# Performance work log

Measured on AMD Instinct MI355X. Metric: run time of the kernel, lower is better.

The kernel has to match this reference:

```python
import jax, jax.numpy as jnp
import numpy as np

NUM_HEADS = 32
NUM_KV_HEADS = 8
HEAD_DIM = 64
GQA_GROUPS = NUM_HEADS // NUM_KV_HEADS
HIDDEN = 2048
B, S = 2, 2048


def setup_inputs() -> dict:
    key = jax.random.key(0)
    ks = jax.random.split(key, 7)
    scale = 1.0 / np.sqrt(HIDDEN)
    return {
        "x": jax.random.normal(ks[0], (B, S, HIDDEN), dtype=jnp.float32),
        "rotary_cos": jax.random.uniform(ks[1], (S, HEAD_DIM // 2), dtype=jnp.float32),
        "rotary_sin": jax.random.uniform(ks[2], (S, HEAD_DIM // 2), dtype=jnp.float32),
        "Wq": jax.random.normal(ks[3], (HIDDEN, NUM_HEADS * HEAD_DIM), dtype=jnp.float32) * scale,
        "Wk": jax.random.normal(ks[4], (HIDDEN, NUM_KV_HEADS * HEAD_DIM), dtype=jnp.float32) * scale,
        "Wv": jax.random.normal(ks[5], (HIDDEN, NUM_KV_HEADS * HEAD_DIM), dtype=jnp.float32) * scale,
        "Wo": jax.random.normal(ks[6], (NUM_HEADS * HEAD_DIM, HIDDEN), dtype=jnp.float32) * scale,
    }


def _apply_rope(x, cos, sin):
    # x: (B, H, S, hd); cos/sin: (S, hd/2)
    d = x.shape[-1] // 2
    x1, x2 = x[..., :d], x[..., d:]
    cos = cos[None, None]  # (1,1,S,hd/2)
    sin = sin[None, None]
    return jnp.concatenate([x1 * cos - x2 * sin, x2 * cos + x1 * sin], axis=-1)


def reference(x, rotary_cos, rotary_sin, Wq, Wk, Wv, Wo):
    b, s, _ = x.shape
    scale = HEAD_DIM ** -0.5
    q = (x @ Wq).reshape(b, s, NUM_HEADS, HEAD_DIM).transpose(0, 2, 1, 3)
    k = (x @ Wk).reshape(b, s, NUM_KV_HEADS, HEAD_DIM).transpose(0, 2, 1, 3)
    v = (x @ Wv).reshape(b, s, NUM_KV_HEADS, HEAD_DIM).transpose(0, 2, 1, 3)
    q = _apply_rope(q, rotary_cos[:s], rotary_sin[:s])
    k = _apply_rope(k, rotary_cos[:s], rotary_sin[:s])
    # GQA: expand kv heads to full head count (repeat each kv head gqa_groups times)
    k = jnp.repeat(k, GQA_GROUPS, axis=1)  # (B, H, S, hd)
    v = jnp.repeat(v, GQA_GROUPS, axis=1)
    attn = jnp.einsum("bhqd,bhkd->bhqk", q, k) * scale
    causal = jnp.triu(jnp.full((s, s), -jnp.inf, dtype=attn.dtype), k=1)
    attn = attn + causal[None, None]
    attn = jax.nn.softmax(attn.astype(jnp.float32), axis=-1).astype(q.dtype)
    out = jnp.einsum("bhqk,bhkd->bhqd", attn, v)
    out = out.transpose(0, 2, 1, 3).reshape(b, s, NUM_HEADS * HEAD_DIM)
    return out @ Wo
```

## Files before the change

kernel.cpp:

```cpp
#include <hip/hip_runtime.h>
#include <cstdint>
#include <cstddef>


typedef _Float16 f16;
typedef _Float16 half8 __attribute__((ext_vector_type(8)));
typedef _Float16 half4 __attribute__((ext_vector_type(4)));
typedef float floatx4 __attribute__((ext_vector_type(4)));

#define NH 32
#define NKV 8
#define HD 64
#define BB 2
#define SS 2048
#define HID 2048

__device__ __forceinline__ float fast_exp2(float x) {
#if __has_builtin(__builtin_amdgcn_exp2f)
  return __builtin_amdgcn_exp2f(x);
#else
  return __expf(x * 0.69314718056f);
#endif
}

__device__ __forceinline__ void async_copy16(const f16* g, f16* l) {
  __builtin_amdgcn_global_load_lds(
      (const __attribute__((address_space(1))) void*)g,
      (__attribute__((address_space(3))) void*)l, 16, 0, 0);
}

__global__ __launch_bounds__(256) void k_prep(const float* __restrict__ x,
                                              const float* __restrict__ Wq,
                                              const float* __restrict__ Wk,
                                              const float* __restrict__ Wv,
                                              const float* __restrict__ Wo,
                                              f16* __restrict__ Xb,
                                              f16* __restrict__ WqT,
                                              f16* __restrict__ WkT,
                                              f16* __restrict__ WvT,
                                              f16* __restrict__ WoT) {
  __shared__ float tile[32][33];
  const int bid = blockIdx.x;
  const int t = threadIdx.x;
  if (bid < 4096) {
    const size_t i = ((size_t)bid * 256 + t) * 8;
    const float4 a = *(const float4*)(x + i);
    const float4 b = *(const float4*)(x + i + 4);
    half8 h;
    h[0] = (f16)a.x; h[1] = (f16)a.y; h[2] = (f16)a.z; h[3] = (f16)a.w;
    h[4] = (f16)b.x; h[5] = (f16)b.y; h[6] = (f16)b.z; h[7] = (f16)b.w;
    *(half8*)(Xb + i) = h;
    return;
  }
  const float* in;
  f16* out;
  int C, l;
  if (bid < 8192)       { in = Wq; out = WqT; C = 2048; l = bid - 4096; }
  else if (bid < 9216)  { in = Wk; out = WkT; C = 512;  l = bid - 8192; }
  else if (bid < 10240) { in = Wv; out = WvT; C = 512;  l = bid - 9216; }
  else                  { in = Wo; out = WoT; C = 2048; l = bid - 10240; }
  const int nx = C >> 5;
  const int c0 = (l % nx) * 32, r0 = (l / nx) * 32;
  const int r = t >> 3;
  const int c4 = (t & 7) * 4;
  const float4 v = *(const float4*)(in + (size_t)(r0 + r) * C + c0 + c4);
  tile[r][c4 + 0] = v.x; tile[r][c4 + 1] = v.y;
  tile[r][c4 + 2] = v.z; tile[r][c4 + 3] = v.w;
  __syncthreads();
  half4 o;
  o[0] = (f16)tile[c4 + 0][r];
  o[1] = (f16)tile[c4 + 1][r];
  o[2] = (f16)tile[c4 + 2][r];
  o[3] = (f16)tile[c4 + 3][r];
  *(half4*)(out + (size_t)(c0 + r) * 2048 + r0 + c4) = o;
}

__global__ __launch_bounds__(256) void k_gemm_qkv(const f16* __restrict__ A,
                                                  const f16* __restrict__ Bt,
                                                  const float* __restrict__ rc,
                                                  const float* __restrict__ rs,
                                                  f16* __restrict__ Qr,
                                                  f16* __restrict__ Kr,
                                                  f16* __restrict__ Vt) {
  __shared__ f16 SMEM[128 * 130];
  f16* As = SMEM;
  f16* Bs = SMEM + 128 * 64;
  const int K = HID;
  const int t = threadIdx.x;
  const int w = t >> 6, lane = t & 63;
  const int m0 = blockIdx.y * 128, n0 = blockIdx.x * 128;
  const int wm = (w >> 1) * 64, wn = (w & 1) * 64;
  const int quad = lane >> 4, col = lane & 15;
  const int srow = lane >> 3;
  const int schunk = (lane & 7) ^ srow;

  floatx4 acc[4][4];
  const floatx4 zero = {0.f, 0.f, 0.f, 0.f};
#pragma unroll
  for (int i = 0; i < 4; ++i)
#pragma unroll
    for (int j = 0; j < 4; ++j) acc[i][j] = zero;

  const f16* Ag = A + (size_t)(m0 + w * 32 + srow) * K + schunk * 8;
  const f16* Bg = Bt + (size_t)(n0 + w * 32 + srow) * K + schunk * 8;
  f16* Al = As + (w * 32) * 64;
  f16* Bl = Bs + (w * 32) * 64;

  for (int k0 = 0; k0 < K; k0 += 64) {
#pragma unroll
    for (int i = 0; i < 4; ++i) {
      async_copy16(Ag + k0 + (size_t)(i * 8) * K, Al + i * 8 * 64);
      async_copy16(Bg + k0 + (size_t)(i * 8) * K, Bl + i * 8 * 64);
    }
    __syncthreads();
    half8 af[2][4], bf[2][4];
#pragma unroll
    for (int kc = 0; kc < 2; ++kc)
#pragma unroll
      for (int i = 0; i < 4; ++i) {
        const int ra = wm + i * 16 + col;
        const int rb = wn + i * 16 + col;
        af[kc][i] = *(const half8*)(As + ra * 64 + ((kc * 4 + quad) ^ (ra & 7)) * 8);
        bf[kc][i] = *(const half8*)(Bs + rb * 64 + ((kc * 4 + quad) ^ (rb & 7)) * 8);
      }
#pragma unroll
    for (int i = 0; i < 4; ++i)
#pragma unroll
      for (int j = 0; j < 4; ++j) {
        acc[i][j] = __builtin_amdgcn_mfma_f32_16x16x32_f16(af[0][i], bf[0][j], acc[i][j], 0, 0, 0);
        acc[i][j] = __builtin_amdgcn_mfma_f32_16x16x32_f16(af[1][i], bf[1][j], acc[i][j], 0, 0, 0);
      }
    __syncthreads();
  }

  const int nblk = blockIdx.x;
  if (nblk < 20) {
    f16* outp;
    int nheads, hh;
    float scale;
    if (nblk < 16) { outp = Qr; nheads = NH; hh = (n0 + wn) >> 6;
                     scale = 0.125f * 1.44269504089f; }
    else           { outp = Kr; nheads = NKV; hh = (n0 - 2048 + wn) >> 6;
                     scale = 1.0f; }
#pragma unroll
    for (int i = 0; i < 4; ++i) {
#pragma unroll
      for (int r = 0; r < 4; ++r) {
        const int sg = m0 + wm + i * 16 + quad * 4 + r;
        const int b = sg >> 11, s = sg & 2047;
        const float c1 = rc[s * 32 + col];
        const float sv1 = rs[s * 32 + col];
        const float c2 = rc[s * 32 + 16 + col];
        const float sv2 = rs[s * 32 + 16 + col];
        f16* op = outp + ((size_t)(b * nheads + hh) * SS + s) * HD;
        const float x1a = acc[i][0][r], x2a = acc[i][2][r];
        op[col]      = (f16)((x1a * c1 - x2a * sv1) * scale);
        op[col + 32] = (f16)((x2a * c1 + x1a * sv1) * scale);
        const float x1b = acc[i][1][r], x2b = acc[i][3][r];
        op[col + 16] = (f16)((x1b * c2 - x2b * sv2) * scale);
        op[col + 48] = (f16)((x2b * c2 + x1b * sv2) * scale);
      }
    }
  } else {
    const int kvb = (n0 - 2560) >> 6;
    const int bb = m0 >> 11;
    const int s0 = m0 & 2047;
#pragma unroll
    for (int i = 0; i < 4; ++i)
#pragma unroll
      for (int j = 0; j < 4; ++j) {
        const int dl = wn + j * 16 + col;
        const int sl = wm + i * 16 + quad * 4;
        half4 pv;
        pv[0] = (f16)acc[i][j][0]; pv[1] = (f16)acc[i][j][1];
        pv[2] = (f16)acc[i][j][2]; pv[3] = (f16)acc[i][j][3];
        *(half4*)(SMEM + dl * 130 + sl) = pv;
      }
    __syncthreads();
    const int dl = t >> 1, hf = t & 1;
    const int kv = kvb + (dl >> 6), d = dl & 63;
    const f16* src = SMEM + dl * 130 + hf * 64;
    f16* vp = Vt + ((size_t)(bb * NKV + kv) * HD + d) * SS + s0 + hf * 64;
#pragma unroll
    for (int cc = 0; cc < 8; ++cc)
      *(uint4*)(vp + cc * 8) = *(const uint4*)(src + cc * 8);
  }
}

__global__ __launch_bounds__(256) void k_gemm(const f16* __restrict__ A,
                                              const f16* __restrict__ Bt,
                                              float* __restrict__ Cf,
                                              int N, int K) {
  __shared__ f16 As[128 * 64];
  __shared__ f16 Bs[128 * 64];
  const int t = threadIdx.x;
  const int w = t >> 6, lane = t & 63;
  const int m0 = blockIdx.y * 128, n0 = blockIdx.x * 128;
  const int wm = (w >> 1) * 64, wn = (w & 1) * 64;
  const int quad = lane >> 4, col = lane & 15;
  const int srow = lane >> 3;
  const int schunk = (lane & 7) ^ srow;

  floatx4 acc[4][4];
  const floatx4 zero = {0.f, 0.f, 0.f, 0.f};
#pragma unroll
  for (int i = 0; i < 4; ++i)
#pragma unroll
    for (int j = 0; j < 4; ++j) acc[i][j] = zero;

  const f16* Ag = A + (size_t)(m0 + w * 32 + srow) * K + schunk * 8;
  const f16* Bg = Bt + (size_t)(n0 + w * 32 + srow) * K + schunk * 8;
  f16* Al = As + (w * 32) * 64;
  f16* Bl = Bs + (w * 32) * 64;

  for (int k0 = 0; k0 < K; k0 += 64) {
#pragma unroll
    for (int i = 0; i < 4; ++i) {
      async_copy16(Ag + k0 + (size_t)(i * 8) * K, Al + i * 8 * 64);
      async_copy16(Bg + k0 + (size_t)(i * 8) * K, Bl + i * 8 * 64);
    }
    __syncthreads();
    half8 af[2][4], bf[2][4];
#pragma unroll
    for (int kc = 0; kc < 2; ++kc)
#pragma unroll
      for (int i = 0; i < 4; ++i) {
        const int ra = wm + i * 16 + col;
        const int rb = wn + i * 16 + col;
        af[kc][i] = *(const half8*)(As + ra * 64 + ((kc * 4 + quad) ^ (ra & 7)) * 8);
        bf[kc][i] = *(const half8*)(Bs + rb * 64 + ((kc * 4 + quad) ^ (rb & 7)) * 8);
      }
#pragma unroll
    for (int i = 0; i < 4; ++i)
#pragma unroll
      for (int j = 0; j < 4; ++j) {
        acc[i][j] = __builtin_amdgcn_mfma_f32_16x16x32_f16(af[0][i], bf[0][j], acc[i][j], 0, 0, 0);
        acc[i][j] = __builtin_amdgcn_mfma_f32_16x16x32_f16(af[1][i], bf[1][j], acc[i][j], 0, 0, 0);
      }
    __syncthreads();
  }
#pragma unroll
  for (int i = 0; i < 4; ++i) {
    const int row0 = m0 + wm + i * 16 + quad * 4;
#pragma unroll
    for (int j = 0; j < 4; ++j) {
      const int cc = n0 + wn + j * 16 + col;
#pragma unroll
      for (int r = 0; r < 4; ++r)
        Cf[(size_t)(row0 + r) * N + cc] = acc[i][j][r];
    }
  }
}

__global__ __launch_bounds__(256, 2) void k_attn(const f16* __restrict__ Qb,
                                                 const f16* __restrict__ Kb,
                                                 const f16* __restrict__ Vg,
                                                 f16* __restrict__ O) {
  __shared__ f16 Ks[2][64 * 64];
  __shared__ f16 Vs[2][64 * 64];
  __shared__ f16 Pl[4][32 * 72];
  const int t = threadIdx.x;
  const int w = t >> 6, lane = t & 63;
  const int quad = lane >> 4, col = lane & 15;
  const int qp = blockIdx.x;
  const int kv = blockIdx.y, b = blockIdx.z;
  const int h = kv * 4 + w;
  f16* P = &Pl[w][0];

  const f16* Qh = Qb + (size_t)(b * NH + h) * SS * HD;
  const f16* Kh = Kb + (size_t)(b * NKV + kv) * SS * HD;
  const f16* Vh = Vg + (size_t)(b * NKV + kv) * HD * SS;

  int sr[2], sl[2];
#pragma unroll
  for (int j = 0; j < 2; ++j) {
    const int flat = t + j * 256;
    sr[j] = flat >> 3;
    sl[j] = (flat & 7) ^ (sr[j] & 7);
  }

  const int cx7 = col & 7;
  const floatx4 zero = {0.f, 0.f, 0.f, 0.f};
  const float M = 10.0f;

#pragma unroll
  for (int tile = 0; tile < 2; ++tile) {
    const int qt = tile ? qp : 63 - qp;
    const int qb = qt * 32;

    half8 qf[2][2];
#pragma unroll
    for (int rt = 0; rt < 2; ++rt)
#pragma unroll
      for (int kc = 0; kc < 2; ++kc)
        qf[rt][kc] = *(const half8*)(Qh + (size_t)(qb + rt * 16 + col) * HD + kc * 32 + quad * 8);

    floatx4 oacc[2][4];
#pragma unroll
    for (int rt = 0; rt < 2; ++rt)
#pragma unroll
      for (int dt = 0; dt < 4; ++dt) oacc[rt][dt] = zero;
    float lrow[2] = {0.f, 0.f};

    const int niter = (qb + 32 + 63) >> 6;

    __syncthreads();
#pragma unroll
    for (int j = 0; j < 2; ++j) {
      async_copy16(Kh + (size_t)sr[j] * HD + sl[j] * 8, &Ks[0][(t + j * 256) * 8]);
      async_copy16(Vh + (size_t)sr[j] * SS + sl[j] * 8, &Vs[0][(t + j * 256) * 8]);
    }

    for (int it = 0; it < niter; ++it) {
      const int kb0 = it << 6;
      __syncthreads();
      if (it + 1 < niter) {
        const int nb = (it + 1) & 1;
        const int kn = kb0 + 64;
#pragma unroll
        for (int j = 0; j < 2; ++j) {
          async_copy16(Kh + (size_t)(kn + sr[j]) * HD + sl[j] * 8, &Ks[nb][(t + j * 256) * 8]);
          async_copy16(Vh + (size_t)sr[j] * SS + kn + sl[j] * 8, &Vs[nb][(t + j * 256) * 8]);
        }
      }
      const f16* Kt = &Ks[it & 1][0];
      const f16* Vtl = &Vs[it & 1][0];

      half8 kf[4][2];
#pragma unroll
      for (int st = 0; st < 4; ++st)
#pragma unroll
        for (int kc = 0; kc < 2; ++kc)
          kf[st][kc] = *(const half8*)(Kt + (st * 16 + col) * 64 + (((kc * 4 + quad) ^ cx7) * 8));

      floatx4 s[2][4];
#pragma unroll
      for (int rt = 0; rt < 2; ++rt)
#pragma unroll
        for (int st = 0; st < 4; ++st) {
          floatx4 a = __builtin_amdgcn_mfma_f32_16x16x32_f16(kf[st][0], qf[rt][0], zero, 0, 0, 0);
          s[rt][st]  = __builtin_amdgcn_mfma_f32_16x16x32_f16(kf[st][1], qf[rt][1], a, 0, 0, 0);
        }

      if (it == niter - 1) {
#pragma unroll
        for (int rt = 0; rt < 2; ++rt) {
          const int qrow = qb + rt * 16 + col;
#pragma unroll
          for (int st = 0; st < 4; ++st)
#pragma unroll
            for (int r = 0; r < 4; ++r)
              if (kb0 + st * 16 + quad * 4 + r > qrow) s[rt][st][r] = -1e30f;
        }
      }

#pragma unroll
      for (int rt = 0; rt < 2; ++rt) {
        float psum = 0.f;
#pragma unroll
        for (int st = 0; st < 4; ++st) {
          const float p0 = fast_exp2(s[rt][st][0] - M);
          const float p1 = fast_exp2(s[rt][st][1] - M);
          const float p2 = fast_exp2(s[rt][st][2] - M);
          const float p3 = fast_exp2(s[rt][st][3] - M);
          psum += (p0 + p1) + (p2 + p3);
          half4 pk;
          pk[0] = (f16)p0; pk[1] = (f16)p1; pk[2] = (f16)p2; pk[3] = (f16)p3;
          *(half4*)(P + (rt * 16 + col) * 72 + st * 16 + quad * 4) = pk;
        }
        psum += __shfl_xor(psum, 16, 64);
        psum += __shfl_xor(psum, 32, 64);
        lrow[rt] += psum;
      }

      __asm__ volatile("s_waitcnt lgkmcnt(0)" ::: "memory");

      half8 vf[4][2], pf[2][2];
#pragma unroll
      for (int dt = 0; dt < 4; ++dt)
#pragma unroll
        for (int kc = 0; kc < 2; ++kc)
          vf[dt][kc] = *(const half8*)(Vtl + (dt * 16 + col) * 64 + (((kc * 4 + quad) ^ cx7) * 8));
#pragma unroll
      for (int rt = 0; rt < 2; ++rt) {
        pf[rt][0] = *(const half8*)(P + (rt * 16 + col) * 72 + quad * 8);
        pf[rt][1] = *(const half8*)(P + (rt * 16 + col) * 72 + 32 + quad * 8);
      }
#pragma unroll
      for (int rt = 0; rt < 2; ++rt)
#pragma unroll
        for (int dt = 0; dt < 4; ++dt) {
          oacc[rt][dt] = __builtin_amdgcn_mfma_f32_16x16x32_f16(vf[dt][0], pf[rt][0], oacc[rt][dt], 0, 0, 0);
          oacc[rt][dt] = __builtin_amdgcn_mfma_f32_16x16x32_f16(vf[dt][1], pf[rt][1], oacc[rt][dt], 0, 0, 0);
        }
    }

#pragma unroll
    for (int rt = 0; rt < 2; ++rt) {
      const float inv = 1.0f / lrow[rt];
      f16* op = O + (size_t)(b * SS + qb + rt * 16 + col) * 2048 + h * 64;
#pragma unroll
      for (int dt = 0; dt < 4; ++dt) {
        half4 ov;
        ov[0] = (f16)(oacc[rt][dt][0] * inv);
        ov[1] = (f16)(oacc[rt][dt][1] * inv);
        ov[2] = (f16)(oacc[rt][dt][2] * inv);
        ov[3] = (f16)(oacc[rt][dt][3] * inv);
        *(half4*)(op + dt * 16 + quad * 4) = ov;
      }
    }
  }
}

extern "C" void kernel_launch(void* const* d_in, const int* in_sizes, int n_in,
                              void* d_out, int out_size, void* d_ws, size_t ws_size,
                              hipStream_t stream) {
  const float* x  = (const float*)d_in[0];
  const float* rc = (const float*)d_in[1];
  const float* rs = (const float*)d_in[2];
  const float* Wq = (const float*)d_in[3];
  const float* Wk = (const float*)d_in[4];
  const float* Wv = (const float*)d_in[5];
  const float* Wo = (const float*)d_in[6];
  float* out = (float*)d_out;

  char* ws = (char*)d_ws;
  f16* Xb  = (f16*)(ws);
  f16* WqT = (f16*)(ws + 16777216);
  f16* WkT = (f16*)(ws + 25165824);
  f16* WvT = (f16*)(ws + 27262976);
  f16* WoT = (f16*)(ws + 29360128);
  f16* Qr  = (f16*)(ws + 62914560);
  f16* Kr  = (f16*)(ws + 79691776);
  f16* Vt  = (f16*)(ws + 83886080);
  f16* O   = Xb;

  k_prep<<<14336, 256, 0, stream>>>(x, Wq, Wk, Wv, Wo, Xb, WqT, WkT, WvT, WoT);
  k_gemm_qkv<<<dim3(24, 32), 256, 0, stream>>>(Xb, WqT, rc, rs, Qr, Kr, Vt);
  k_attn<<<dim3(32, NKV, BB), 256, 0, stream>>>(Qr, Kr, Vt, O);
  k_gemm<<<dim3(16, 32), 256, 0, stream>>>(O, WoT, out, 2048, HID);
}
```

Measured before the change: 289.0 us.

## Rewrite projection GEMMs as 256x256 double-buffered 8-wave tiles with interleaved prefetch

Both the QKV and output-projection GEMMs now share a core that computes 256x256 tiles with 512 threads. It double-buffers shared memory and issues the next K-tile's async copies in quarters between MFMA groups, with manual waitcnt and barriers and raised wave priority around the MFMAs. Block IDs are swizzled to improve L2 reuse. The larger tiles cut global reloads, but the grid shrinks to 192 and 128 blocks, which may underfill the 256 CUs. The 128 KB of shared memory per block also limits occupancy.

```diff
diff --git a/kernel.cpp b/kernel.cpp
--- a/kernel.cpp
+++ b/kernel.cpp
@@ -75,78 +75,147 @@
   *(half4*)(out + (size_t)(c0 + r) * 2048 + r0 + c4) = o;
 }
 
-__global__ __launch_bounds__(256) void k_gemm_qkv(const f16* __restrict__ A,
-                                                  const f16* __restrict__ Bt,
-                                                  const float* __restrict__ rc,
-                                                  const float* __restrict__ rs,
-                                                  f16* __restrict__ Qr,
-                                                  f16* __restrict__ Kr,
-                                                  f16* __restrict__ Vt) {
-  __shared__ f16 SMEM[128 * 130];
-  f16* As = SMEM;
-  f16* Bs = SMEM + 128 * 64;
-  const int K = HID;
+__device__ __forceinline__ void core256(const f16* __restrict__ A,
+                                        const f16* __restrict__ Bt,
+                                        const int K, const int m0, const int n0,
+                                        f16* __restrict__ SM,
+                                        floatx4 (&acc)[8][4]) {
   const int t = threadIdx.x;
   const int w = t >> 6, lane = t & 63;
-  const int m0 = blockIdx.y * 128, n0 = blockIdx.x * 128;
-  const int wm = (w >> 1) * 64, wn = (w & 1) * 64;
+  const int wr = w >> 2, wc = w & 3;
   const int quad = lane >> 4, col = lane & 15;
-  const int srow = lane >> 3;
-  const int schunk = (lane & 7) ^ srow;
-
-  floatx4 acc[4][4];
+  const int nkt = K >> 6;
+
+  f16* const Ab0 = SM;
+  f16* const Ab1 = SM + 16384;
+  f16* const Bb0 = SM + 32768;
+  f16* const Bb1 = SM + 49152;
+
+  const int srow = t >> 3;
+  const int schunk = (t & 7) ^ (srow & 7);
+  const f16* const Asrc = A + (size_t)(m0 + srow) * K + schunk * 8;
+  const f16* const Bsrc = Bt + (size_t)(n0 + srow) * K + schunk * 8;
+  const int ldst = w * 512;
+
   const floatx4 zero = {0.f, 0.f, 0.f, 0.f};
 #pragma unroll
-  for (int i = 0; i < 4; ++i)
+  for (int i = 0; i < 8; ++i)
 #pragma unroll
     for (int j = 0; j < 4; ++j) acc[i][j] = zero;
 
-  const f16* Ag = A + (size_t)(m0 + w * 32 + srow) * K + schunk * 8;
-  const f16* Bg = Bt + (size_t)(n0 + w * 32 + srow) * K + schunk * 8;
-  f16* Al = As + (w * 32) * 64;
-  f16* Bl = Bs + (w * 32) * 64;
-
-  for (int k0 = 0; k0 < K; k0 += 64) {
-#pragma unroll
-    for (int i = 0; i < 4; ++i) {
-      async_copy16(Ag + k0 + (size_t)(i * 8) * K, Al + i * 8 * 64);
-      async_copy16(Bg + k0 + (size_t)(i * 8) * K, Bl + i * 8 * 64);
-    }
-    __syncthreads();
-    half8 af[2][4], bf[2][4];
-#pragma unroll
-    for (int kc = 0; kc < 2; ++kc)
-#pragma unroll
-      for (int i = 0; i < 4; ++i) {
-        const int ra = wm + i * 16 + col;
-        const int rb = wn + i * 16 + col;
-        af[kc][i] = *(const half8*)(As + ra * 64 + ((kc * 4 + quad) ^ (ra & 7)) * 8);
-        bf[kc][i] = *(const half8*)(Bs + rb * 64 + ((kc * 4 + quad) ^ (rb & 7)) * 8);
-      }
-#pragma unroll
-    for (int i = 0; i < 4; ++i)
-#pragma unroll
-      for (int j = 0; j < 4; ++j) {
-        acc[i][j] = __builtin_amdgcn_mfma_f32_16x16x32_f16(af[0][i], bf[0][j], acc[i][j], 0, 0, 0);
-        acc[i][j] = __builtin_amdgcn_mfma_f32_16x16x32_f16(af[1][i], bf[1][j], acc[i][j], 0, 0, 0);
-      }
-    __syncthreads();
-  }
-
-  const int nblk = blockIdx.x;
-  if (nblk < 20) {
+#pragma unroll
+  for (int r = 0; r < 4; ++r) {
+    async_copy16(Asrc + (size_t)(r * 64) * K, Ab0 + r * 4096 + ldst);
+    async_copy16(Bsrc + (size_t)(r * 64) * K, Bb0 + r * 4096 + ldst);
+  }
+  __asm__ volatile("s_waitcnt vmcnt(0)" ::: "memory");
+  __builtin_amdgcn_s_barrier();
+
+  for (int kt = 0; kt < nkt; ++kt) {
+    const f16* const Ac = (kt & 1) ? Ab1 : Ab0;
+    const f16* const Bc = (kt & 1) ? Bb1 : Bb0;
+    f16* const An = (kt & 1) ? Ab0 : Ab1;
+    f16* const Bn = (kt & 1) ? Bb0 : Bb1;
+    const bool pf = (kt + 1 < nkt);
+    const f16* const Apf = Asrc + (size_t)(kt + 1) * 64;
+    const f16* const Bpf = Bsrc + (size_t)(kt + 1) * 64;
+    half8 bf[4][2];
+#pragma unroll
+    for (int q = 0; q < 4; ++q) {
+      if (q == 0) {
+#pragma unroll
+        for (int j = 0; j < 4; ++j) {
+          const int rb = wc * 64 + j * 16 + col;
+#pragma unroll
+          for (int kc = 0; kc < 2; ++kc)
+            bf[j][kc] = *(const half8*)(Bc + rb * 64 +
+                                        (((kc * 4 + quad) ^ (rb & 7)) * 8));
+        }
+      }
+      half8 af[2][2];
+#pragma unroll
+      for (int ii = 0; ii < 2; ++ii) {
+        const int ra = wr * 128 + (q * 2 + ii) * 16 + col;
+#pragma unroll
+        for (int kc = 0; kc < 2; ++kc)
+          af[ii][kc] = *(const half8*)(Ac + ra * 64 +
+                                       (((kc * 4 + quad) ^ (ra & 7)) * 8));
+      }
+      if (pf) {
+        if (q == 0) {
+          async_copy16(Bpf, Bn + ldst);
+          async_copy16(Bpf + (size_t)64 * K, Bn + 4096 + ldst);
+        } else if (q == 1) {
+          async_copy16(Bpf + (size_t)128 * K, Bn + 8192 + ldst);
+          async_copy16(Bpf + (size_t)192 * K, Bn + 12288 + ldst);
+        } else if (q == 2) {
+          async_copy16(Apf, An + ldst);
+          async_copy16(Apf + (size_t)128 * K, An + 8192 + ldst);
+        } else {
+          async_copy16(Apf + (size_t)64 * K, An + 4096 + ldst);
+          async_copy16(Apf + (size_t)192 * K, An + 12288 + ldst);
+        }
+      }
+      __builtin_amdgcn_s_barrier();
+      __asm__ volatile("s_waitcnt lgkmcnt(0)" ::: "memory");
+      __builtin_amdgcn_sched_barrier(0);
+      __builtin_amdgcn_s_setprio(1);
+#pragma unroll
+      for (int ii = 0; ii < 2; ++ii)
+#pragma unroll
+        for (int j = 0; j < 4; ++j) {
+          acc[q * 2 + ii][j] = __builtin_amdgcn_mfma_f32_16x16x32_f16(
+              af[ii][0], bf[j][0], acc[q * 2 + ii][j], 0, 0, 0);
+          acc[q * 2 + ii][j] = __builtin_amdgcn_mfma_f32_16x16x32_f16(
+              af[ii][1], bf[j][1], acc[q * 2 + ii][j], 0, 0, 0);
+        }
+      __builtin_amdgcn_s_setprio(0);
+      if (q == 1) {
+        if (pf) __asm__ volatile("s_waitcnt vmcnt(4)" ::: "memory");
+        else    __asm__ volatile("s_waitcnt vmcnt(0)" ::: "memory");
+      }
+      if (q == 3 && pf) {
+        __asm__ volatile("s_waitcnt vmcnt(2)" ::: "memory");
+      }
+      __builtin_amdgcn_s_barrier();
+    }
+  }
+}
+
+__global__ __launch_bounds__(512, 2) void k_gemm_qkv(const f16* __restrict__ A,
+                                                     const f16* __restrict__ Bt,
+                                                     const float* __restrict__ rc,
+                                                     const float* __restrict__ rs,
+                                                     f16* __restrict__ Qr,
+                                                     f16* __restrict__ Kr,
+                                                     f16* __restrict__ Vt) {
+  __shared__ f16 SM[65536];
+  const int bid = blockIdx.x;
+  const int swz = (bid & 7) * 24 + (bid >> 3);
+  const int nt = swz % 12, mt = swz / 12;
+  const int m0 = mt * 256, n0 = nt * 256;
+
+  floatx4 acc[8][4];
+  core256(A, Bt, HID, m0, n0, SM, acc);
+
+  const int t = threadIdx.x;
+  const int w = t >> 6, lane = t & 63;
+  const int wr = w >> 2, wc = w & 3;
+  const int quad = lane >> 4, col = lane & 15;
+
+  if (nt < 10) {
     f16* outp;
     int nheads, hh;
     float scale;
-    if (nblk < 16) { outp = Qr; nheads = NH; hh = (n0 + wn) >> 6;
-                     scale = 0.125f * 1.44269504089f; }
-    else           { outp = Kr; nheads = NKV; hh = (n0 - 2048 + wn) >> 6;
-                     scale = 1.0f; }
-#pragma unroll
-    for (int i = 0; i < 4; ++i) {
+    if (nt < 8) { outp = Qr; nheads = NH; hh = (n0 + wc * 64) >> 6;
+                  scale = 0.125f * 1.44269504089f; }
+    else        { outp = Kr; nheads = NKV; hh = (n0 - 2048 + wc * 64) >> 6;
+                  scale = 1.0f; }
+#pragma unroll
+    for (int i = 0; i < 8; ++i) {
 #pragma unroll
       for (int r = 0; r < 4; ++r) {
-        const int sg = m0 + wm + i * 16 + quad * 4 + r;
+        const int sg = m0 + wr * 128 + i * 16 + quad * 4 + r;
         const int b = sg >> 11, s = sg & 2047;
         const float c1 = rc[s * 32 + col];
         const float sv1 = rs[s * 32 + col];
@@ -162,89 +231,62 @@
       }
     }
   } else {
-    const int kvb = (n0 - 2560) >> 6;
+    const int kv0 = (n0 - 2560) >> 6;
     const int bb = m0 >> 11;
     const int s0 = m0 & 2047;
 #pragma unroll
-    for (int i = 0; i < 4; ++i)
-#pragma unroll
-      for (int j = 0; j < 4; ++j) {
-        const int dl = wn + j * 16 + col;
-        const int sl = wm + i * 16 + quad * 4;
-        half4 pv;
-        pv[0] = (f16)acc[i][j][0]; pv[1] = (f16)acc[i][j][1];
-        pv[2] = (f16)acc[i][j][2]; pv[3] = (f16)acc[i][j][3];
-        *(half4*)(SMEM + dl * 130 + sl) = pv;
-      }
-    __syncthreads();
-    const int dl = t >> 1, hf = t & 1;
-    const int kv = kvb + (dl >> 6), d = dl & 63;
-    const f16* src = SMEM + dl * 130 + hf * 64;
-    f16* vp = Vt + ((size_t)(bb * NKV + kv) * HD + d) * SS + s0 + hf * 64;
-#pragma unroll
-    for (int cc = 0; cc < 8; ++cc)
-      *(uint4*)(vp + cc * 8) = *(const uint4*)(src + cc * 8);
-  }
-}
-
-__global__ __launch_bounds__(256) void k_gemm(const f16* __restrict__ A,
-                                              const f16* __restrict__ Bt,
-                                              float* __restrict__ Cf,
-                                              int N, int K) {
-  __shared__ f16 As[128 * 64];
-  __shared__ f16 Bs[128 * 64];
+    for (int hs = 0; hs < 2; ++hs) {
+      __builtin_amdgcn_s_barrier();
+      if (wr == hs) {
+#pragma unroll
+        for (int i = 0; i < 8; ++i)
+#pragma unroll
+          for (int j = 0; j < 4; ++j) {
+            const int dl = wc * 64 + j * 16 + col;
+            const int sl = i * 16 + quad * 4;
+            half4 pv;
+            pv[0] = (f16)acc[i][j][0]; pv[1] = (f16)acc[i][j][1];
+            pv[2] = (f16)acc[i][j][2]; pv[3] = (f16)acc[i][j][3];
+            *(half4*)(SM + dl * 136 + sl) = pv;
+          }
+      }
+      __builtin_amdgcn_s_barrier();
+#pragma unroll
+      for (int rr = 0; rr < 8; ++rr) {
+        const int flat = t + rr * 512;
+        const int dl = flat >> 4, s8 = (flat & 15) * 8;
+        const int kv = kv0 + (dl >> 6), d = dl & 63;
+        f16* vp = Vt + ((size_t)(bb * NKV + kv) * HD + d) * SS + s0 +
+                  hs * 128 + s8;
+        *(uint4*)vp = *(const uint4*)(SM + dl * 136 + s8);
+      }
+    }
+  }
+}
+
+__global__ __launch_bounds__(512, 2) void k_gemm(const f16* __restrict__ A,
+                                                 const f16* __restrict__ Bt,
+                                                 float* __restrict__ Cf,
+                                                 int N, int K) {
+  __shared__ f16 SM[65536];
+  const int bid = blockIdx.x;
+  const int swz = (bid & 7) * 16 + (bid >> 3);
+  const int nt = swz & 7, mt = swz >> 3;
+  const int m0 = mt * 256, n0 = nt * 256;
+
+  floatx4 acc[8][4];
+  core256(A, Bt, K, m0, n0, SM, acc);
+
   const int t = threadIdx.x;
   const int w = t >> 6, lane = t & 63;
-  const int m0 = blockIdx.y * 128, n0 = blockIdx.x * 128;
-  const int wm = (w >> 1) * 64, wn = (w & 1) * 64;
+  const int wr = w >> 2, wc = w & 3;
   const int quad = lane >> 4, col = lane & 15;
-  const int srow = lane >> 3;
-  const int schunk = (lane & 7) ^ srow;
-
-  floatx4 acc[4][4];
-  const floatx4 zero = {0.f, 0.f, 0.f, 0.f};
-#pragma unroll
-  for (int i = 0; i < 4; ++i)
-#pragma unroll
-    for (int j = 0; j < 4; ++j) acc[i][j] = zero;
-
-  const f16* Ag = A + (size_t)(m0 + w * 32 + srow) * K + schunk * 8;
-  const f16* Bg = Bt + (size_t)(n0 + w * 32 + srow) * K + schunk * 8;
-  f16* Al = As + (w * 32) * 64;
-  f16* Bl = Bs + (w * 32) * 64;
-
-  for (int k0 = 0; k0 < K; k0 += 64) {
-#pragma unroll
-    for (int i = 0; i < 4; ++i) {
-      async_copy16(Ag + k0 + (size_t)(i * 8) * K, Al + i * 8 * 64);
-      async_copy16(Bg + k0 + (size_t)(i * 8) * K, Bl + i * 8 * 64);
-    }
-    __syncthreads();
-    half8 af[2][4], bf[2][4];
-#pragma unroll
-    for (int kc = 0; kc < 2; ++kc)
-#pragma unroll
-      for (int i = 0; i < 4; ++i) {
-        const int ra = wm + i * 16 + col;
-        const int rb = wn + i * 16 + col;
-        af[kc][i] = *(const half8*)(As + ra * 64 + ((kc * 4 + quad) ^ (ra & 7)) * 8);
-        bf[kc][i] = *(const half8*)(Bs + rb * 64 + ((kc * 4 + quad) ^ (rb & 7)) * 8);
-      }
-#pragma unroll
-    for (int i = 0; i < 4; ++i)
-#pragma unroll
-      for (int j = 0; j < 4; ++j) {
-        acc[i][j] = __builtin_amdgcn_mfma_f32_16x16x32_f16(af[0][i], bf[0][j], acc[i][j], 0, 0, 0);
-        acc[i][j] = __builtin_amdgcn_mfma_f32_16x16x32_f16(af[1][i], bf[1][j], acc[i][j], 0, 0, 0);
-      }
-    __syncthreads();
-  }
-#pragma unroll
-  for (int i = 0; i < 4; ++i) {
-    const int row0 = m0 + wm + i * 16 + quad * 4;
+#pragma unroll
+  for (int i = 0; i < 8; ++i) {
+    const int row0 = m0 + wr * 128 + i * 16 + quad * 4;
 #pragma unroll
     for (int j = 0; j < 4; ++j) {
-      const int cc = n0 + wn + j * 16 + col;
+      const int cc = n0 + wc * 64 + j * 16 + col;
 #pragma unroll
       for (int r = 0; r < 4; ++r)
         Cf[(size_t)(row0 + r) * N + cc] = acc[i][j][r];
@@ -436,7 +478,7 @@
   f16* O   = Xb;
 
   k_prep<<<14336, 256, 0, stream>>>(x, Wq, Wk, Wv, Wo, Xb, WqT, WkT, WvT, WoT);
-  k_gemm_qkv<<<dim3(24, 32), 256, 0, stream>>>(Xb, WqT, rc, rs, Qr, Kr, Vt);
+  k_gemm_qkv<<<192, 512, 0, stream>>>(Xb, WqT, rc, rs, Qr, Kr, Vt);
   k_attn<<<dim3(32, NKV, BB), 256, 0, stream>>>(Qr, Kr, Vt, O);
-  k_gemm<<<dim3(16, 32), 256, 0, stream>>>(O, WoT, out, 2048, HID);
-}
+  k_gemm<<<128, 512, 0, stream>>>(O, WoT, out, 2048, HID);
+}
```

Result: slower. 294.9 us (+2.0%).
